# Kernel optimization log

Hardware: AMD Instinct MI355X
Metric: run time of the kernel (lower is better)

## Reference

```python
import jax, jax.numpy as jnp
import numpy as np
import math
from jax import lax

L, E, H, F = 4, 1024, 16, 4096
B, S = 8, 512
VV, VR = 40, 30
DIST_V = 200
PAD_ID = 0


def setup_inputs() -> dict:
    key = jax.random.key(0)
    ks = iter(jax.random.split(key, 32))
    w = lambda *sh: jax.random.normal(next(ks), sh, jnp.float32) * 0.02
    inp = {
        'val_emb': w(VV, E),
        'ring_emb': w(VR, E),
        'dist_emb': w(DIST_V, H),
        'Wqkv': w(L, 3 * E, E), 'bqkv': jnp.zeros((L, 3 * E), jnp.float32),
        'Wo': w(L, E, E), 'bo': jnp.zeros((L, E), jnp.float32),
        'ln1_s': jnp.ones((L, E), jnp.float32), 'ln1_b': jnp.zeros((L, E), jnp.float32),
        'W1': w(L, F, E), 'b1': jnp.zeros((L, F), jnp.float32),
        'W2': w(L, E, F), 'b2': jnp.zeros((L, E), jnp.float32),
        'ln2_s': jnp.ones((L, E), jnp.float32), 'ln2_b': jnp.zeros((L, E), jnp.float32),
        'lnf_s': jnp.ones((E,), jnp.float32), 'lnf_b': jnp.zeros((E,), jnp.float32),
        'gen_W': w(VV * VR, E), 'gen_b': jnp.zeros((VV * VR,), jnp.float32),
    }
    val = jax.random.randint(next(ks), (B, S), 0, VV)
    val = val.at[:, 0].set(1)  # ensure first key is never <pad> (id 0)
    inp['val_sequences'] = val
    inp['ring_sequences'] = jax.random.randint(next(ks), (B, S), 0, VR)
    inp['distance_squares'] = jax.random.randint(next(ks), (B, S, S), 0, DIST_V)
    return inp


def _ln(x, s, b):
    m = x.mean(-1, keepdims=True)
    v = ((x - m) ** 2).mean(-1, keepdims=True)
    return (x - m) / jnp.sqrt(v + 1e-5) * s + b


def _forward(val_emb, ring_emb, dist_emb, Wqkv, bqkv, Wo, bo, ln1_s, ln1_b,
             W1, b1, W2, b2, ln2_s, ln2_b, lnf_s, lnf_b, gen_W, gen_b,
             val_sequences, ring_sequences, distance_squares):
    Bv, Sv = val_sequences.shape
    dh = E // H
    scale = 1.0 / math.sqrt(dh)
    # token embeddings, each scaled by sqrt(emb_size)
    x = (val_emb[val_sequences] + ring_emb[ring_sequences]) * math.sqrt(E)  # [B,S,E]
    # distance bias [B,S,S,H] -> [B,H,S,S], causal fill with -inf, key padding -inf
    bias = jnp.transpose(dist_emb[distance_squares], (0, 3, 1, 2))
    causal = jnp.tril(jnp.ones((Sv, Sv), bool))
    mask = jnp.where(causal[None, None], bias, -jnp.inf)
    pad = (val_sequences == PAD_ID)  # [B,S]
    mask = jnp.where(pad[:, None, None, :], -jnp.inf, mask)

    def step(h, p):
        wqkv, bq, wo, bo_, l1s, l1b, w1, b1_, w2, b2_, l2s, l2b = p
        qkv = h @ wqkv.T + bq  # [B,S,3E]
        q, k, v = jnp.split(qkv, 3, axis=-1)
        q = q.reshape(Bv, Sv, H, dh).transpose(0, 2, 1, 3)
        k = k.reshape(Bv, Sv, H, dh).transpose(0, 2, 1, 3)
        v = v.reshape(Bv, Sv, H, dh).transpose(0, 2, 1, 3)
        scores = jnp.einsum('bhqd,bhkd->bhqk', q, k) * scale + mask
        a = jax.nn.softmax(scores, axis=-1)
        ctx = jnp.einsum('bhqk,bhkd->bhqd', a, v)
        ctx = ctx.transpose(0, 2, 1, 3).reshape(Bv, Sv, E)
        h = _ln(h + ctx @ wo.T + bo_, l1s, l1b)  # post-norm
        ff = jax.nn.gelu(h @ w1.T + b1_, approximate=False) @ w2.T + b2_
        h = _ln(h + ff, l2s, l2b)
        return h, None

    layer_params = (Wqkv, bqkv, Wo, bo, ln1_s, ln1_b, W1, b1, W2, b2, ln2_s, ln2_b)
    x, _ = lax.scan(step, x, layer_params)
    x = _ln(x, lnf_s, lnf_b)
    return x @ gen_W.T + gen_b  # [B,S,VV*VR]


def reference(val_emb, ring_emb, dist_emb, Wqkv, bqkv, Wo, bo, ln1_s, ln1_b,
              W1, b1, W2, b2, ln2_s, ln2_b, lnf_s, lnf_b, gen_W, gen_b,
              val_sequences, ring_sequences, distance_squares):
    return _forward(val_emb, ring_emb, dist_emb, Wqkv, bqkv, Wo, bo, ln1_s, ln1_b,
                    W1, b1, W2, b2, ln2_s, ln2_b, lnf_s, lnf_b, gen_W, gen_b,
                    val_sequences, ring_sequences, distance_squares)
```

## Files before the change

kernel.cpp:

```cpp
#include <hip/hip_runtime.h>
#include <hip/hip_bf16.h>

typedef __attribute__((ext_vector_type(8))) short bf16x8;
typedef __attribute__((ext_vector_type(4))) float f32x4;
typedef unsigned short u16;
typedef __attribute__((ext_vector_type(4))) unsigned short u16x4;

#define L_ 4
#define E_ 1024
#define H_ 16
#define F_ 4096
#define B_ 8
#define S_ 512
#define T_ 4096
#define GEN_N 1200
#define GEN_PAD 1280

#define AS1 __attribute__((address_space(1)))
#define AS3 __attribute__((address_space(3)))

static __device__ __forceinline__ u16 f2bf(float f) {
  unsigned u = __float_as_uint(f);
  unsigned r = (u + 0x7fffu + ((u >> 16) & 1u)) >> 16;
  return (u16)r;
}

static __device__ __forceinline__ unsigned cvt_pk_bf16(float lo, float hi) {
  unsigned r;
  asm("v_cvt_pk_bf16_f32 %0, %1, %2" : "=v"(r) : "v"(lo), "v"(hi));
  return r;
}

static __device__ __forceinline__ float fast_gelu(float v) {
  float y = 0.7978845608f * (v + 0.044715f * v * v * v);
  y = fminf(fmaxf(y, -9.f), 9.f);
  float e2 = __expf(2.f * y);
  float th = (e2 - 1.f) / (e2 + 1.f);
  return 0.5f * v * (1.f + th);
}

__global__ __launch_bounds__(256) void cvt_bf16(const float* __restrict__ src,
                                                u16* __restrict__ dst, int n) {
  int i = (blockIdx.x * 256 + threadIdx.x) * 4;
  if (i >= n) return;
  float4 v = *reinterpret_cast<const float4*>(src + i);
  u16x4 o = {f2bf(v.x), f2bf(v.y), f2bf(v.z), f2bf(v.w)};
  *reinterpret_cast<u16x4*>(dst + i) = o;
}

__global__ __launch_bounds__(256) void embed_k(const float* __restrict__ val_emb,
                                               const float* __restrict__ ring_emb,
                                               const int* __restrict__ vseq,
                                               const int* __restrict__ rseq,
                                               float* __restrict__ h, u16* __restrict__ xbf) {
  int tok = blockIdx.x;
  int e = threadIdx.x * 4;
  int v = vseq[tok], r = rseq[tok];
  float4 a = *reinterpret_cast<const float4*>(val_emb + v * E_ + e);
  float4 b = *reinterpret_cast<const float4*>(ring_emb + r * E_ + e);
  float4 o;
  o.x = (a.x + b.x) * 32.f; o.y = (a.y + b.y) * 32.f;
  o.z = (a.z + b.z) * 32.f; o.w = (a.w + b.w) * 32.f;
  *reinterpret_cast<float4*>(h + (size_t)tok * E_ + e) = o;
  u16x4 ob = {f2bf(o.x), f2bf(o.y), f2bf(o.z), f2bf(o.w)};
  *reinterpret_cast<u16x4*>(xbf + (size_t)tok * E_ + e) = ob;
}

__global__ __launch_bounds__(256) void ln_k(const float* hin, const float* add0,
                                            const float* add1, const float* cbias,
                                            const float* g, const float* bta,
                                            float* hout, u16* xout) {
  int tok = blockIdx.x;
  int e = threadIdx.x * 4;
  float4 v = *reinterpret_cast<const float4*>(hin + (size_t)tok * E_ + e);
  if (add0) {
    float4 a0 = *reinterpret_cast<const float4*>(add0 + (size_t)tok * E_ + e);
    float4 a1 = *reinterpret_cast<const float4*>(add1 + (size_t)tok * E_ + e);
    float4 cb = *reinterpret_cast<const float4*>(cbias + e);
    v.x += a0.x + a1.x + cb.x; v.y += a0.y + a1.y + cb.y;
    v.z += a0.z + a1.z + cb.z; v.w += a0.w + a1.w + cb.w;
  }
  float s = v.x + v.y + v.z + v.w;
  float q = v.x * v.x + v.y * v.y + v.z * v.z + v.w * v.w;
  #pragma unroll
  for (int off = 1; off < 64; off <<= 1) {
    s += __shfl_xor(s, off, 64);
    q += __shfl_xor(q, off, 64);
  }
  __shared__ float ls[4], lq[4];
  int wv = threadIdx.x >> 6, ln = threadIdx.x & 63;
  if (ln == 0) { ls[wv] = s; lq[wv] = q; }
  __syncthreads();
  s = ls[0] + ls[1] + ls[2] + ls[3];
  q = lq[0] + lq[1] + lq[2] + lq[3];
  float mean = s * (1.f / E_);
  float var = q * (1.f / E_) - mean * mean;
  float inv = rsqrtf(var + 1e-5f);
  float4 gg = *reinterpret_cast<const float4*>(g + e);
  float4 bb = *reinterpret_cast<const float4*>(bta + e);
  float4 o;
  o.x = (v.x - mean) * inv * gg.x + bb.x;
  o.y = (v.y - mean) * inv * gg.y + bb.y;
  o.z = (v.z - mean) * inv * gg.z + bb.z;
  o.w = (v.w - mean) * inv * gg.w + bb.w;
  if (hout) *reinterpret_cast<float4*>(hout + (size_t)tok * E_ + e) = o;
  u16x4 ob = {f2bf(o.x), f2bf(o.y), f2bf(o.z), f2bf(o.w)};
  *reinterpret_cast<u16x4*>(xout + (size_t)tok * E_ + e) = ob;
}

template <int EPI, int NW, int SPLITK>
__global__ __launch_bounds__(512, 2) void gemm_big(const u16* __restrict__ A,
                                                   const u16* __restrict__ W,
                                                   const float* __restrict__ bias,
                                                   void* __restrict__ Cp,
                                                   u16* __restrict__ Vt,
                                                   int M, int N, int K, int tilesN) {
  constexpr int BN = 64 * NW;
  __shared__ __align__(16) u16 As[2][256 * 64];
  __shared__ __align__(16) u16 Bs[2][BN * 64];
  int tid = threadIdx.x;
  int wid = tid >> 6, ln = tid & 63;
  int wm = wid >> 2, wn = wid & 3;
  int lr = ln & 15, lk = ln >> 4;
  int nwg = gridDim.x;
  int bid = blockIdx.x;
  int swz = ((nwg & 7) == 0) ? ((bid & 7) * (nwg >> 3) + (bid >> 3)) : bid;
  int sp = 0, tile = swz;
  if (SPLITK > 1) { sp = swz & (SPLITK - 1); tile = swz / SPLITK; }
  int tm = tile / tilesN, tn = tile % tilesN;
  int row0 = tm * 256, col0 = tn * BN;
  int Ks = K / SPLITK;
  int kbase = sp * Ks;

  int srow = tid >> 3;
  int schunk = ((tid & 7) ^ (srow & 7)) * 8;
  const u16* gA = A + (size_t)(row0 + srow) * K + kbase + schunk;
  const u16* gB = W + (size_t)(col0 + srow) * K + kbase + schunk;
  size_t ldsBase = (size_t)((wid << 3) * 64) * 2;

  auto stage = [&](int buf, int kt) {
    size_t ko = (size_t)kt * 64;
    #pragma unroll
    for (int i = 0; i < 4; ++i)
      __builtin_amdgcn_global_load_lds(
          (const AS1 void*)(gA + (size_t)i * 64 * K + ko),
          (AS3 void*)((char*)&As[buf][0] + ldsBase + (size_t)i * 64 * 128), 16, 0, 0);
    #pragma unroll
    for (int i = 0; i < NW; ++i)
      __builtin_amdgcn_global_load_lds(
          (const AS1 void*)(gB + (size_t)i * 64 * K + ko),
          (AS3 void*)((char*)&Bs[buf][0] + ldsBase + (size_t)i * 64 * 128), 16, 0, 0);
  };

  f32x4 acc[8][NW];
  f32x4 z = {0.f, 0.f, 0.f, 0.f};
  #pragma unroll
  for (int m = 0; m < 8; ++m)
    #pragma unroll
    for (int n = 0; n < NW; ++n) acc[m][n] = z;

  auto compute = [&](int buf) {
    #pragma unroll
    for (int s = 0; s < 2; ++s) {
      int ch = ((s * 4 + lk) ^ (lr & 7)) * 8;
      bf16x8 bfr[NW];
      #pragma unroll
      for (int n = 0; n < NW; ++n)
        bfr[n] = *reinterpret_cast<const bf16x8*>(&Bs[buf][(wn * (16 * NW) + n * 16 + lr) * 64 + ch]);
      #pragma unroll
      for (int m = 0; m < 8; ++m) {
        bf16x8 af = *reinterpret_cast<const bf16x8*>(&As[buf][(wm * 128 + m * 16 + lr) * 64 + ch]);
        #pragma unroll
        for (int n = 0; n < NW; ++n)
          acc[m][n] = __builtin_amdgcn_mfma_f32_16x16x32_bf16(af, bfr[n], acc[m][n], 0, 0, 0);
      }
    }
  };

  int nt = Ks >> 6;
  stage(0, 0);
  int cur = 0;
  for (int t = 0; t < nt; ++t) {
    if (t + 1 < nt) {
      stage(cur ^ 1, t + 1);
      if constexpr (NW == 2) asm volatile("s_waitcnt vmcnt(6)" ::: "memory");
      else if constexpr (NW == 3) asm volatile("s_waitcnt vmcnt(7)" ::: "memory");
      else asm volatile("s_waitcnt vmcnt(8)" ::: "memory");
    } else {
      asm volatile("s_waitcnt vmcnt(0)" ::: "memory");
    }
    __builtin_amdgcn_s_barrier();
    asm volatile("" ::: "memory");
    compute(cur);
    asm volatile("" ::: "memory");
    __builtin_amdgcn_s_barrier();
    cur ^= 1;
  }

  #pragma unroll
  for (int n = 0; n < NW; ++n) {
    int col = col0 + wn * (16 * NW) + n * 16 + lr;
    if (col >= N) continue;
    float bv = (EPI == 2) ? 0.f : bias[col];
    #pragma unroll
    for (int m = 0; m < 8; ++m) {
      int rbase = row0 + wm * 128 + m * 16 + lk * 4;
      #pragma unroll
      for (int r2 = 0; r2 < 4; ++r2) {
        float v = acc[m][n][r2] + bv;
        if (EPI == 1) v = fast_gelu(v);
        int row = rbase + r2;
        if (EPI == 2)
          ((float*)Cp)[(size_t)sp * M * N + (size_t)row * N + col] = v;
        else if (EPI == 3)
          ((float*)Cp)[(size_t)row * N + col] = v;
        else {
          u16 bw = f2bf(v);
          ((u16*)Cp)[(size_t)row * N + col] = bw;
          if (EPI == 0 && Vt != nullptr && col >= 2 * E_) {
            int dg = col - 2 * E_;
            int hh = dg >> 6, dd = dg & 63;
            int bb = row >> 9, ss = row & 511;
            Vt[((size_t)((bb * 16 + hh) * 64 + dd) << 9) + ss] = bw;
          }
        }
      }
    }
  }
}

__global__ __launch_bounds__(256, 4) void attn_fused_k(const u16* __restrict__ qkv,
                                                       const int* __restrict__ dist,
                                                       const float* __restrict__ dist_emb,
                                                       const int* __restrict__ vseq,
                                                       const u16* __restrict__ Vt,
                                                       u16* __restrict__ ctx) {
  int blk = blockIdx.x;
  int bh = blk & 127;
  int qt = blk >> 7;
  int b = bh >> 4, h = bh & 15;
  int tid = threadIdx.x, wv = tid >> 6, l = tid & 63;
  int lr = l & 15, lk = l >> 4;

  __shared__ float de[208];
  __shared__ unsigned char padf[512];
  __shared__ unsigned char d8[64 * 516];

  int ncol = (qt + 1) * 64;
  for (int i = tid; i < 208; i += 256)
    de[i] = (i < 200) ? dist_emb[i * H_ + h] : -1e30f;
  for (int i = tid; i < (ncol >> 2); i += 256) {
    int4 v = *reinterpret_cast<const int4*>(vseq + b * S_ + i * 4);
    uchar4 pz;
    pz.x = (v.x == 0); pz.y = (v.y == 0); pz.z = (v.z == 0); pz.w = (v.w == 0);
    *reinterpret_cast<uchar4*>(&padf[i * 4]) = pz;
  }
  __syncthreads();

  {
    int r = tid >> 2;
    const int* drow = dist + ((size_t)(b * S_ + qt * 64 + r) << 9);
    int nc4 = ncol >> 2;
    for (int c4 = (tid & 3); c4 < nc4; c4 += 4) {
      int4 dv = *reinterpret_cast<const int4*>(drow + c4 * 4);
      uchar4 o;
      o.x = padf[c4 * 4 + 0] ? (unsigned char)200 : (unsigned char)dv.x;
      o.y = padf[c4 * 4 + 1] ? (unsigned char)200 : (unsigned char)dv.y;
      o.z = padf[c4 * 4 + 2] ? (unsigned char)200 : (unsigned char)dv.z;
      o.w = padf[c4 * 4 + 3] ? (unsigned char)200 : (unsigned char)dv.w;
      *reinterpret_cast<uchar4*>(&d8[r * 516 + c4 * 4]) = o;
    }
  }
  __syncthreads();

  int q0 = qt * 64 + wv * 16;
  int nv = 4 * qt + wv + 1;
  int qglob = q0 + lr;
  int qloc = wv * 16 + lr;

  bf16x8 aq0 = *reinterpret_cast<const bf16x8*>(
      qkv + (size_t)(b * S_ + q0 + lr) * 3072 + h * 64 + lk * 8);
  bf16x8 aq1 = *reinterpret_cast<const bf16x8*>(
      qkv + (size_t)(b * S_ + q0 + lr) * 3072 + h * 64 + 32 + lk * 8);

  float sm = 0.f;
  f32x4 z = {0.f, 0.f, 0.f, 0.f};
  f32x4 acc_o[4] = {z, z, z, z};

  int sA = lr + ((2 * lk) & 3) * 16;
  int sB = lr + ((2 * lk + 1) & 3) * 16;
  int jsel = (lk >= 2);

  int ngroups = (nv + 1) >> 1;
  #pragma unroll 1
  for (int g = 0; g < ngroups; ++g) {
    f32x4 s0 = z, s1 = z;
    {
      int n = 2 * g;
      const u16* kb = qkv + (size_t)(b * S_ + n * 16 + lr) * 3072 + E_ + h * 64 + lk * 8;
      bf16x8 bk0 = *reinterpret_cast<const bf16x8*>(kb);
      bf16x8 bk1 = *reinterpret_cast<const bf16x8*>(kb + 32);
      s0 = __builtin_amdgcn_mfma_f32_16x16x32_bf16(bk0, aq0, s0, 0, 0, 0);
      s0 = __builtin_amdgcn_mfma_f32_16x16x32_bf16(bk1, aq1, s0, 0, 0, 0);
    }
    if (2 * g + 1 < nv) {
      int n = 2 * g + 1;
      const u16* kb = qkv + (size_t)(b * S_ + n * 16 + lr) * 3072 + E_ + h * 64 + lk * 8;
      bf16x8 bk0 = *reinterpret_cast<const bf16x8*>(kb);
      bf16x8 bk1 = *reinterpret_cast<const bf16x8*>(kb + 32);
      s1 = __builtin_amdgcn_mfma_f32_16x16x32_bf16(bk0, aq0, s1, 0, 0, 0);
      s1 = __builtin_amdgcn_mfma_f32_16x16x32_bf16(bk1, aq1, s1, 0, 0, 0);
    }
    float e0[4], e1[4];
    #pragma unroll
    for (int r2 = 0; r2 < 4; ++r2) {
      int kg0 = (2 * g) * 16 + lk * 4 + r2;
      float e = 0.f;
      if (kg0 <= qglob) {
        int d = d8[qloc * 516 + kg0];
        e = __expf(s0[r2] * 0.125f + de[d]);
      }
      e0[r2] = e; sm += e;
    }
    #pragma unroll
    for (int r2 = 0; r2 < 4; ++r2) {
      int kg1 = (2 * g + 1) * 16 + lk * 4 + r2;
      float e = 0.f;
      if (2 * g + 1 < nv && kg1 <= qglob) {
        int d = d8[qloc * 516 + kg1];
        e = __expf(s1[r2] * 0.125f + de[d]);
      }
      e1[r2] = e; sm += e;
    }
    unsigned t0p0 = cvt_pk_bf16(e0[0], e0[1]);
    unsigned t0p1 = cvt_pk_bf16(e0[2], e0[3]);
    unsigned t1p0 = cvt_pk_bf16(e1[0], e1[1]);
    unsigned t1p1 = cvt_pk_bf16(e1[2], e1[3]);
    unsigned a00 = __shfl((int)t0p0, sA, 64), a10 = __shfl((int)t1p0, sA, 64);
    unsigned a01 = __shfl((int)t0p1, sA, 64), a11 = __shfl((int)t1p1, sA, 64);
    unsigned b00 = __shfl((int)t0p0, sB, 64), b10 = __shfl((int)t1p0, sB, 64);
    unsigned b01 = __shfl((int)t0p1, sB, 64), b11 = __shfl((int)t1p1, sB, 64);
    unsigned w0 = jsel ? a10 : a00;
    unsigned w1 = jsel ? a11 : a01;
    unsigned w2 = jsel ? b10 : b00;
    unsigned w3 = jsel ? b11 : b01;
    bf16x8 pfrag;
    {
      unsigned pw[4] = {w0, w1, w2, w3};
      pfrag = *reinterpret_cast<bf16x8*>(pw);
    }
    #pragma unroll
    for (int n4 = 0; n4 < 4; ++n4) {
      bf16x8 vf = *reinterpret_cast<const bf16x8*>(
          Vt + (size_t)(bh * 64 + n4 * 16 + lr) * S_ + g * 32 + lk * 8);
      acc_o[n4] = __builtin_amdgcn_mfma_f32_16x16x32_bf16(vf, pfrag, acc_o[n4], 0, 0, 0);
    }
  }

  sm += __shfl_xor(sm, 16, 64);
  sm += __shfl_xor(sm, 32, 64);
  float il = 1.f / sm;

  #pragma unroll
  for (int n4 = 0; n4 < 4; ++n4) {
    u16x4 o;
    o.x = f2bf(acc_o[n4][0] * il);
    o.y = f2bf(acc_o[n4][1] * il);
    o.z = f2bf(acc_o[n4][2] * il);
    o.w = f2bf(acc_o[n4][3] * il);
    *reinterpret_cast<u16x4*>(ctx + (size_t)(b * S_ + qglob) * E_ + h * 64 + n4 * 16 + lk * 4) = o;
  }
}

extern "C" void kernel_launch(void* const* d_in, const int* in_sizes, int n_in,
                              void* d_out, int out_size, void* d_ws, size_t ws_size,
                              hipStream_t stream) {
  const float* val_emb = (const float*)d_in[0];
  const float* ring_emb = (const float*)d_in[1];
  const float* dist_emb = (const float*)d_in[2];
  const float* Wqkv = (const float*)d_in[3];
  const float* bqkv = (const float*)d_in[4];
  const float* Wo = (const float*)d_in[5];
  const float* bo = (const float*)d_in[6];
  const float* ln1_s = (const float*)d_in[7];
  const float* ln1_b = (const float*)d_in[8];
  const float* W1 = (const float*)d_in[9];
  const float* b1 = (const float*)d_in[10];
  const float* W2 = (const float*)d_in[11];
  const float* b2 = (const float*)d_in[12];
  const float* ln2_s = (const float*)d_in[13];
  const float* ln2_b = (const float*)d_in[14];
  const float* lnf_s = (const float*)d_in[15];
  const float* lnf_b = (const float*)d_in[16];
  const float* gen_W = (const float*)d_in[17];
  const float* gen_b = (const float*)d_in[18];
  const int* vseq = (const int*)d_in[19];
  const int* rseq = (const int*)d_in[20];
  const int* dist = (const int*)d_in[21];

  char* ws = (char*)d_ws;
  size_t off = 0;
  auto alloc = [&](size_t nbytes) {
    char* p = ws + off;
    off += (nbytes + 255) & ~(size_t)255;
    return p;
  };
  u16* gw_bf = (u16*)alloc((size_t)GEN_PAD * E_ * 2);
  u16* wqkv_l = (u16*)alloc((size_t)3 * E_ * E_ * 2);
  u16* wo_l = (u16*)alloc((size_t)E_ * E_ * 2);
  u16* w1_l = (u16*)alloc((size_t)F_ * E_ * 2);
  u16* w2_l = (u16*)alloc((size_t)E_ * F_ * 2);
  float* h = (float*)alloc((size_t)T_ * E_ * 4);
  u16* x_bf = (u16*)alloc((size_t)T_ * E_ * 2);
  u16* qkv_bf = (u16*)alloc((size_t)T_ * 3 * E_ * 2);
  u16* ctx_bf = (u16*)alloc((size_t)T_ * E_ * 2);
  u16* vt_bf = (u16*)alloc((size_t)B_ * H_ * 64 * S_ * 2);
  u16* p_bf = (u16*)alloc((size_t)B_ * H_ * S_ * S_ * 2);
  u16* ff_bf = p_bf;
  float* psum = (float*)(p_bf + (size_t)T_ * F_);
  (void)ws_size; (void)in_sizes; (void)n_in; (void)out_size; (void)rseq;

  auto cvt = [&](const float* s, u16* d, int n) {
    cvt_bf16<<<dim3((n / 4 + 255) / 256), dim3(256), 0, stream>>>(s, d, n);
  };
  cvt(gen_W, gw_bf, GEN_N * E_);

  embed_k<<<dim3(T_), dim3(256), 0, stream>>>(val_emb, ring_emb, vseq, rseq, h, x_bf);

  for (int l = 0; l < L_; ++l) {
    cvt(Wqkv + (size_t)l * 3 * E_ * E_, wqkv_l, 3 * E_ * E_);
    cvt(Wo + (size_t)l * E_ * E_, wo_l, E_ * E_);
    cvt(W1 + (size_t)l * F_ * E_, w1_l, F_ * E_);
    cvt(W2 + (size_t)l * E_ * F_, w2_l, E_ * F_);

    gemm_big<0, 3, 1><<<dim3(256), dim3(512), 0, stream>>>(
        x_bf, wqkv_l, bqkv + (size_t)l * 3 * E_, qkv_bf, vt_bf, T_, 3 * E_, E_, 16);
    attn_fused_k<<<dim3(B_ * H_ * 8), dim3(256), 0, stream>>>(qkv_bf, dist, dist_emb,
                                                              vseq, vt_bf, ctx_bf);
    gemm_big<2, 2, 2><<<dim3(256), dim3(512), 0, stream>>>(
        ctx_bf, wo_l, nullptr, psum, nullptr, T_, E_, E_, 8);
    ln_k<<<dim3(T_), dim3(256), 0, stream>>>(h, psum, psum + (size_t)T_ * E_,
                                             bo + (size_t)l * E_,
                                             ln1_s + (size_t)l * E_, ln1_b + (size_t)l * E_,
                                             h, x_bf);
    gemm_big<1, 4, 1><<<dim3(256), dim3(512), 0, stream>>>(
        x_bf, w1_l, b1 + (size_t)l * F_, ff_bf, nullptr, T_, F_, E_, 16);
    gemm_big<2, 2, 2><<<dim3(256), dim3(512), 0, stream>>>(
        ff_bf, w2_l, nullptr, psum, nullptr, T_, E_, F_, 8);
    ln_k<<<dim3(T_), dim3(256), 0, stream>>>(h, psum, psum + (size_t)T_ * E_,
                                             b2 + (size_t)l * E_,
                                             ln2_s + (size_t)l * E_, ln2_b + (size_t)l * E_,
                                             h, x_bf);
  }
  ln_k<<<dim3(T_), dim3(256), 0, stream>>>(h, nullptr, nullptr, nullptr, lnf_s, lnf_b,
                                           nullptr, x_bf);
  gemm_big<3, 2, 1><<<dim3(160), dim3(512), 0, stream>>>(
      x_bf, gw_bf, gen_b, (float*)d_out, nullptr, T_, GEN_N, E_, 10);
}
```

Before: 1.086 ms.

## Add smaller-tile GEMM for QKV/FFN1, batch weight casts, wave-per-token layernorm

Adds a 256-thread GEMM with 128x256 tiles and K-step 32 for the QKV and FFN1 projections, replacing the 512-thread 256-row kernel. It aims for more workgroups and better occupancy. The four per-layer weight casts are merged into one launch to cut launch overhead. LayerNorm now runs one wave per token with shuffle-only reductions, which removes the LDS sync. The smaller K-step doubles the number of barriers per tile, and the QKV grid of 384 workgroups may leave a partial wave of blocks.

```diff
diff --git a/kernel.cpp b/kernel.cpp
--- a/kernel.cpp
+++ b/kernel.cpp
@@ -46,6 +46,26 @@
   float4 v = *reinterpret_cast<const float4*>(src + i);
   u16x4 o = {f2bf(v.x), f2bf(v.y), f2bf(v.z), f2bf(v.w)};
   *reinterpret_cast<u16x4*>(dst + i) = o;
+}
+
+__global__ __launch_bounds__(256) void cvt4_k(const float* __restrict__ s0,
+                                              const float* __restrict__ s1,
+                                              const float* __restrict__ s2,
+                                              const float* __restrict__ s3,
+                                              u16* __restrict__ d0, u16* __restrict__ d1,
+                                              u16* __restrict__ d2, u16* __restrict__ d3) {
+  int q = blockIdx.x * 256 + threadIdx.x;
+  const float* s;
+  u16* d;
+  int i;
+  if (q < 786432) { s = s0; d = d0; i = q; }
+  else if (q < 786432 + 262144) { s = s1; d = d1; i = q - 786432; }
+  else if (q < 786432 + 262144 + 1048576) { s = s2; d = d2; i = q - (786432 + 262144); }
+  else { s = s3; d = d3; i = q - (786432 + 262144 + 1048576); }
+  i *= 4;
+  float4 v = *reinterpret_cast<const float4*>(s + i);
+  u16x4 o = {f2bf(v.x), f2bf(v.y), f2bf(v.z), f2bf(v.w)};
+  *reinterpret_cast<u16x4*>(d + i) = o;
 }
 
 __global__ __launch_bounds__(256) void embed_k(const float* __restrict__ val_emb,
@@ -70,42 +90,152 @@
                                             const float* add1, const float* cbias,
                                             const float* g, const float* bta,
                                             float* hout, u16* xout) {
-  int tok = blockIdx.x;
-  int e = threadIdx.x * 4;
-  float4 v = *reinterpret_cast<const float4*>(hin + (size_t)tok * E_ + e);
-  if (add0) {
-    float4 a0 = *reinterpret_cast<const float4*>(add0 + (size_t)tok * E_ + e);
-    float4 a1 = *reinterpret_cast<const float4*>(add1 + (size_t)tok * E_ + e);
-    float4 cb = *reinterpret_cast<const float4*>(cbias + e);
-    v.x += a0.x + a1.x + cb.x; v.y += a0.y + a1.y + cb.y;
-    v.z += a0.z + a1.z + cb.z; v.w += a0.w + a1.w + cb.w;
-  }
-  float s = v.x + v.y + v.z + v.w;
-  float q = v.x * v.x + v.y * v.y + v.z * v.z + v.w * v.w;
+  int tok = blockIdx.x * 4 + (threadIdx.x >> 6);
+  int lane = threadIdx.x & 63;
+  const float* hp = hin + (size_t)tok * E_;
+  float4 v[4];
+  #pragma unroll
+  for (int p = 0; p < 4; ++p) {
+    int e = p * 256 + lane * 4;
+    v[p] = *reinterpret_cast<const float4*>(hp + e);
+    if (add0) {
+      float4 a0 = *reinterpret_cast<const float4*>(add0 + (size_t)tok * E_ + e);
+      float4 a1 = *reinterpret_cast<const float4*>(add1 + (size_t)tok * E_ + e);
+      float4 cb = *reinterpret_cast<const float4*>(cbias + e);
+      v[p].x += a0.x + a1.x + cb.x; v[p].y += a0.y + a1.y + cb.y;
+      v[p].z += a0.z + a1.z + cb.z; v[p].w += a0.w + a1.w + cb.w;
+    }
+  }
+  float s = 0.f, q = 0.f;
+  #pragma unroll
+  for (int p = 0; p < 4; ++p) {
+    s += v[p].x + v[p].y + v[p].z + v[p].w;
+    q += v[p].x * v[p].x + v[p].y * v[p].y + v[p].z * v[p].z + v[p].w * v[p].w;
+  }
   #pragma unroll
   for (int off = 1; off < 64; off <<= 1) {
     s += __shfl_xor(s, off, 64);
     q += __shfl_xor(q, off, 64);
   }
-  __shared__ float ls[4], lq[4];
-  int wv = threadIdx.x >> 6, ln = threadIdx.x & 63;
-  if (ln == 0) { ls[wv] = s; lq[wv] = q; }
-  __syncthreads();
-  s = ls[0] + ls[1] + ls[2] + ls[3];
-  q = lq[0] + lq[1] + lq[2] + lq[3];
   float mean = s * (1.f / E_);
   float var = q * (1.f / E_) - mean * mean;
   float inv = rsqrtf(var + 1e-5f);
-  float4 gg = *reinterpret_cast<const float4*>(g + e);
-  float4 bb = *reinterpret_cast<const float4*>(bta + e);
-  float4 o;
-  o.x = (v.x - mean) * inv * gg.x + bb.x;
-  o.y = (v.y - mean) * inv * gg.y + bb.y;
-  o.z = (v.z - mean) * inv * gg.z + bb.z;
-  o.w = (v.w - mean) * inv * gg.w + bb.w;
-  if (hout) *reinterpret_cast<float4*>(hout + (size_t)tok * E_ + e) = o;
-  u16x4 ob = {f2bf(o.x), f2bf(o.y), f2bf(o.z), f2bf(o.w)};
-  *reinterpret_cast<u16x4*>(xout + (size_t)tok * E_ + e) = ob;
+  #pragma unroll
+  for (int p = 0; p < 4; ++p) {
+    int e = p * 256 + lane * 4;
+    float4 gg = *reinterpret_cast<const float4*>(g + e);
+    float4 bb = *reinterpret_cast<const float4*>(bta + e);
+    float4 o;
+    o.x = (v[p].x - mean) * inv * gg.x + bb.x;
+    o.y = (v[p].y - mean) * inv * gg.y + bb.y;
+    o.z = (v[p].z - mean) * inv * gg.z + bb.z;
+    o.w = (v[p].w - mean) * inv * gg.w + bb.w;
+    if (hout) *reinterpret_cast<float4*>(hout + (size_t)tok * E_ + e) = o;
+    u16x4 ob = {f2bf(o.x), f2bf(o.y), f2bf(o.z), f2bf(o.w)};
+    *reinterpret_cast<u16x4*>(xout + (size_t)tok * E_ + e) = ob;
+  }
+}
+
+template <int EPI>
+__global__ __launch_bounds__(256, 2) void gemm_small(const u16* __restrict__ A,
+                                                     const u16* __restrict__ W,
+                                                     const float* __restrict__ bias,
+                                                     void* __restrict__ Cp,
+                                                     u16* __restrict__ Vt,
+                                                     int M, int N, int K, int tilesN) {
+  __shared__ __align__(16) char lds[49152];
+  int tid = threadIdx.x;
+  int wid = tid >> 6, l = tid & 63;
+  int wm = wid >> 1, wn = wid & 1;
+  int lr = l & 15, lk = l >> 4;
+  int nwg = gridDim.x, bid = blockIdx.x;
+  int swz = ((nwg & 7) == 0) ? ((bid & 7) * (nwg >> 3) + (bid >> 3)) : bid;
+  int tm = swz / tilesN, tn = swz % tilesN;
+  int row0 = tm * 128, col0 = tn * 256;
+
+  int srow = tid >> 2;
+  int sch = ((tid & 3) ^ ((srow >> 1) & 3)) * 8;
+  const u16* gA = A + (size_t)(row0 + srow) * K + sch;
+  const u16* gB = W + (size_t)(col0 + srow) * K + sch;
+  int wslot = wid * 1024;
+
+  auto stage = [&](int buf, int kt) {
+    size_t ko = (size_t)kt * 32;
+    int base = buf * 24576;
+    #pragma unroll
+    for (int i = 0; i < 2; ++i)
+      __builtin_amdgcn_global_load_lds((const AS1 void*)(gA + (size_t)i * 64 * K + ko),
+                                       (AS3 void*)(lds + base + i * 4096 + wslot), 16, 0, 0);
+    #pragma unroll
+    for (int i = 0; i < 4; ++i)
+      __builtin_amdgcn_global_load_lds((const AS1 void*)(gB + (size_t)i * 64 * K + ko),
+                                       (AS3 void*)(lds + base + 8192 + i * 4096 + wslot), 16, 0, 0);
+  };
+
+  int ck = (lk ^ ((lr >> 1) & 3)) * 16;
+  f32x4 acc[4][8];
+  f32x4 z = {0.f, 0.f, 0.f, 0.f};
+  #pragma unroll
+  for (int m = 0; m < 4; ++m)
+    #pragma unroll
+    for (int n = 0; n < 8; ++n) acc[m][n] = z;
+
+  auto compute = [&](int buf) {
+    int base = buf * 24576;
+    bf16x8 bfr[8];
+    #pragma unroll
+    for (int n = 0; n < 8; ++n)
+      bfr[n] = *reinterpret_cast<const bf16x8*>(lds + base + 8192 + (wn * 128 + n * 16 + lr) * 64 + ck);
+    #pragma unroll
+    for (int m = 0; m < 4; ++m) {
+      bf16x8 af = *reinterpret_cast<const bf16x8*>(lds + base + (wm * 64 + m * 16 + lr) * 64 + ck);
+      #pragma unroll
+      for (int n = 0; n < 8; ++n)
+        acc[m][n] = __builtin_amdgcn_mfma_f32_16x16x32_bf16(af, bfr[n], acc[m][n], 0, 0, 0);
+    }
+  };
+
+  int nt = K >> 5;
+  stage(0, 0);
+  int cur = 0;
+  for (int t = 0; t < nt; ++t) {
+    if (t + 1 < nt) {
+      stage(cur ^ 1, t + 1);
+      asm volatile("s_waitcnt vmcnt(6)" ::: "memory");
+    } else {
+      asm volatile("s_waitcnt vmcnt(0)" ::: "memory");
+    }
+    __builtin_amdgcn_s_barrier();
+    asm volatile("" ::: "memory");
+    compute(cur);
+    asm volatile("" ::: "memory");
+    __builtin_amdgcn_s_barrier();
+    cur ^= 1;
+  }
+
+  #pragma unroll
+  for (int n = 0; n < 8; ++n) {
+    int col = col0 + wn * 128 + n * 16 + lr;
+    float bv = bias[col];
+    #pragma unroll
+    for (int m = 0; m < 4; ++m) {
+      int rbase = row0 + wm * 64 + m * 16 + lk * 4;
+      #pragma unroll
+      for (int r2 = 0; r2 < 4; ++r2) {
+        float v = acc[m][n][r2] + bv;
+        if (EPI == 1) v = fast_gelu(v);
+        int row = rbase + r2;
+        u16 bw = f2bf(v);
+        ((u16*)Cp)[(size_t)row * N + col] = bw;
+        if (EPI == 0 && Vt != nullptr && col >= 2 * E_) {
+          int dg = col - 2 * E_;
+          int hh = dg >> 6, dd = dg & 63;
+          int bb = row >> 9, ss = row & 511;
+          Vt[((size_t)((bb * 16 + hh) * 64 + dd) << 9) + ss] = bw;
+        }
+      }
+    }
+  }
 }
 
 template <int EPI, int NW, int SPLITK>
@@ -113,7 +243,6 @@
                                                    const u16* __restrict__ W,
                                                    const float* __restrict__ bias,
                                                    void* __restrict__ Cp,
-                                                   u16* __restrict__ Vt,
                                                    int M, int N, int K, int tilesN) {
   constexpr int BN = 64 * NW;
   __shared__ __align__(16) u16 As[2][256 * 64];
@@ -208,22 +337,11 @@
       #pragma unroll
       for (int r2 = 0; r2 < 4; ++r2) {
         float v = acc[m][n][r2] + bv;
-        if (EPI == 1) v = fast_gelu(v);
         int row = rbase + r2;
         if (EPI == 2)
           ((float*)Cp)[(size_t)sp * M * N + (size_t)row * N + col] = v;
-        else if (EPI == 3)
+        else
           ((float*)Cp)[(size_t)row * N + col] = v;
-        else {
-          u16 bw = f2bf(v);
-          ((u16*)Cp)[(size_t)row * N + col] = bw;
-          if (EPI == 0 && Vt != nullptr && col >= 2 * E_) {
-            int dg = col - 2 * E_;
-            int hh = dg >> 6, dd = dg & 63;
-            int bb = row >> 9, ss = row & 511;
-            Vt[((size_t)((bb * 16 + hh) * 64 + dd) << 9) + ss] = bw;
-          }
-        }
       }
     }
   }
@@ -420,40 +538,37 @@
   float* psum = (float*)(p_bf + (size_t)T_ * F_);
   (void)ws_size; (void)in_sizes; (void)n_in; (void)out_size; (void)rseq;
 
-  auto cvt = [&](const float* s, u16* d, int n) {
-    cvt_bf16<<<dim3((n / 4 + 255) / 256), dim3(256), 0, stream>>>(s, d, n);
-  };
-  cvt(gen_W, gw_bf, GEN_N * E_);
-
+  cvt_bf16<<<dim3((GEN_N * E_ / 4 + 255) / 256), dim3(256), 0, stream>>>(gen_W, gw_bf,
+                                                                         GEN_N * E_);
   embed_k<<<dim3(T_), dim3(256), 0, stream>>>(val_emb, ring_emb, vseq, rseq, h, x_bf);
 
   for (int l = 0; l < L_; ++l) {
-    cvt(Wqkv + (size_t)l * 3 * E_ * E_, wqkv_l, 3 * E_ * E_);
-    cvt(Wo + (size_t)l * E_ * E_, wo_l, E_ * E_);
-    cvt(W1 + (size_t)l * F_ * E_, w1_l, F_ * E_);
-    cvt(W2 + (size_t)l * E_ * F_, w2_l, E_ * F_);
-
-    gemm_big<0, 3, 1><<<dim3(256), dim3(512), 0, stream>>>(
-        x_bf, wqkv_l, bqkv + (size_t)l * 3 * E_, qkv_bf, vt_bf, T_, 3 * E_, E_, 16);
+    cvt4_k<<<dim3(12288), dim3(256), 0, stream>>>(
+        Wqkv + (size_t)l * 3 * E_ * E_, Wo + (size_t)l * E_ * E_,
+        W1 + (size_t)l * F_ * E_, W2 + (size_t)l * E_ * F_,
+        wqkv_l, wo_l, w1_l, w2_l);
+
+    gemm_small<0><<<dim3(384), dim3(256), 0, stream>>>(
+        x_bf, wqkv_l, bqkv + (size_t)l * 3 * E_, qkv_bf, vt_bf, T_, 3 * E_, E_, 12);
     attn_fused_k<<<dim3(B_ * H_ * 8), dim3(256), 0, stream>>>(qkv_bf, dist, dist_emb,
                                                               vseq, vt_bf, ctx_bf);
     gemm_big<2, 2, 2><<<dim3(256), dim3(512), 0, stream>>>(
-        ctx_bf, wo_l, nullptr, psum, nullptr, T_, E_, E_, 8);
-    ln_k<<<dim3(T_), dim3(256), 0, stream>>>(h, psum, psum + (size_t)T_ * E_,
-                                             bo + (size_t)l * E_,
-                                             ln1_s + (size_t)l * E_, ln1_b + (size_t)l * E_,
-                                             h, x_bf);
-    gemm_big<1, 4, 1><<<dim3(256), dim3(512), 0, stream>>>(
+        ctx_bf, wo_l, nullptr, psum, T_, E_, E_, 8);
+    ln_k<<<dim3(T_ / 4), dim3(256), 0, stream>>>(h, psum, psum + (size_t)T_ * E_,
+                                                 bo + (size_t)l * E_,
+                                                 ln1_s + (size_t)l * E_, ln1_b + (size_t)l * E_,
+                                                 h, x_bf);
+    gemm_small<1><<<dim3(512), dim3(256), 0, stream>>>(
         x_bf, w1_l, b1 + (size_t)l * F_, ff_bf, nullptr, T_, F_, E_, 16);
     gemm_big<2, 2, 2><<<dim3(256), dim3(512), 0, stream>>>(
-        ff_bf, w2_l, nullptr, psum, nullptr, T_, E_, F_, 8);
-    ln_k<<<dim3(T_), dim3(256), 0, stream>>>(h, psum, psum + (size_t)T_ * E_,
-                                             b2 + (size_t)l * E_,
-                                             ln2_s + (size_t)l * E_, ln2_b + (size_t)l * E_,
-                                             h, x_bf);
-  }
-  ln_k<<<dim3(T_), dim3(256), 0, stream>>>(h, nullptr, nullptr, nullptr, lnf_s, lnf_b,
-                                           nullptr, x_bf);
+        ff_bf, w2_l, nullptr, psum, T_, E_, F_, 8);
+    ln_k<<<dim3(T_ / 4), dim3(256), 0, stream>>>(h, psum, psum + (size_t)T_ * E_,
+                                                 b2 + (size_t)l * E_,
+                                                 ln2_s + (size_t)l * E_, ln2_b + (size_t)l * E_,
+                                                 h, x_bf);
+  }
+  ln_k<<<dim3(T_ / 4), dim3(256), 0, stream>>>(h, nullptr, nullptr, nullptr, lnf_s, lnf_b,
+                                               nullptr, x_bf);
   gemm_big<3, 2, 1><<<dim3(160), dim3(512), 0, stream>>>(
-      x_bf, gw_bf, gen_b, (float*)d_out, nullptr, T_, GEN_N, E_, 10);
-}
+      x_bf, gw_bf, gen_b, (float*)d_out, T_, GEN_N, E_, 10);
+}
```

Measured after the change: 1.047 ms. 3.6% less time.
